# Kernel tuning notes

Hardware: AMD Instinct MI355X
Metric: run time of the kernel (lower is better)

The kernel has to match this reference:

```python
import jax, jax.numpy as jnp
import numpy as np

THETA = 0.5  # forward default arg
ALPHA = 0.2  # LeakyReLU negative slope
NEG_INF = -9e15


def setup_inputs() -> dict:
    key = jax.random.key(0)
    k1, k2, k3, k4, k5 = jax.random.split(key, 5)
    N, F_IN, F_OUT = 8192, 256, 256
    h = jax.random.normal(k1, (N, F_IN), dtype=jnp.float32)
    adj = jax.random.randint(k2, (N, N), 0, 2, dtype=jnp.int32)
    cv_values = jax.random.uniform(k3, (N,), dtype=jnp.float32)
    # xavier_uniform with gain=1.414
    g = 1.414
    bw = g * np.sqrt(6.0 / (F_IN + F_OUT))
    W = jax.random.uniform(k4, (F_IN, F_OUT), dtype=jnp.float32, minval=-bw, maxval=bw)
    ba = g * np.sqrt(6.0 / (2 * F_OUT + 1))
    a = jax.random.uniform(k5, (2 * F_OUT, 1), dtype=jnp.float32, minval=-ba, maxval=ba)
    return {"h": h, "adj": adj, "cv_values": cv_values, "W": W, "a": a}


def reference(h, adj, cv_values, W, a):
    # Wh: [N, F_out]
    Wh = h @ W
    F_out = Wh.shape[1]
    a1 = a[:F_out, 0]   # [F_out]
    a2 = a[F_out:, 0]   # [F_out]
    # e_ij = LeakyReLU([Wh_i ; Wh_j] . a) = LeakyReLU(Wh_i.a1 + Wh_j.a2)
    f1 = Wh @ a1        # [N]
    f2 = Wh @ a2        # [N]
    e = jax.nn.leaky_relu(f1[:, None] + f2[None, :], negative_slope=ALPHA)
    # CV bias: theta * cv_i broadcast across row i
    e = e + THETA * cv_values[:, None]
    att = jnp.where(adj > 0, e, jnp.float32(NEG_INF))
    att = jax.nn.softmax(att, axis=1)
    # dropout is identity in eval mode (training=False)
    h_prime = att @ Wh  # [N, F_out]
    return jax.nn.elu(h_prime)  # concat=True branch
```

## Files before the change

### kernel.cpp

```cpp
#include <hip/hip_runtime.h>
#include <cstdint>
#include <cstddef>

typedef _Float16 half8 __attribute__((ext_vector_type(8)));
typedef _Float16 half4 __attribute__((ext_vector_type(4)));
typedef float f32x4 __attribute__((ext_vector_type(4)));

#define GAT_N 8192
#define GAT_F 256
#define GAT_ALPHA 0.2f
#define GAT_LOG2E 1.4426950408889634f

__device__ inline unsigned enc_f32(float x) {
    unsigned b = __float_as_uint(x);
    return (b & 0x80000000u) ? ~b : (b | 0x80000000u);
}
__device__ inline float dec_f32(unsigned u) {
    unsigned b = (u & 0x80000000u) ? (u ^ 0x80000000u) : ~u;
    return __uint_as_float(b);
}

__global__ __launch_bounds__(256) void gat_k0_convert(
    const float* __restrict__ h, const float* __restrict__ W,
    _Float16* __restrict__ h16, _Float16* __restrict__ WT,
    unsigned* __restrict__ f2mxEnc)
{
    const int gtid = blockIdx.x * 256 + threadIdx.x;
    if (gtid == 0) *f2mxEnc = 0u;
    for (int i = gtid; i < (GAT_N * GAT_F / 4); i += 131072) {
        float4 v = reinterpret_cast<const float4*>(h)[i];
        half4 o; o[0] = (_Float16)v.x; o[1] = (_Float16)v.y;
        o[2] = (_Float16)v.z; o[3] = (_Float16)v.w;
        reinterpret_cast<half4*>(h16)[i] = o;
    }
    if (gtid < GAT_F * GAT_F) {
        int k = gtid >> 8, n = gtid & 255;
        WT[n * GAT_F + k] = (_Float16)W[gtid];
    }
}

__global__ __launch_bounds__(256) void gat_k1_gemm(
    const _Float16* __restrict__ h16, const _Float16* __restrict__ WT,
    const float* __restrict__ a, _Float16* __restrict__ whT,
    float* __restrict__ f1, float* __restrict__ f2,
    unsigned* __restrict__ f2mxEnc)
{
    const int wv = threadIdx.x >> 6;
    const int lane = threadIdx.x & 63;
    const int l15 = lane & 15;
    const int quad = lane >> 4;
    const int r0 = blockIdx.x * 64 + wv * 16;

    f32x4 acc[16];
    #pragma unroll
    for (int t = 0; t < 16; ++t) { f32x4 z = {0.f,0.f,0.f,0.f}; acc[t] = z; }

    #pragma unroll
    for (int k0 = 0; k0 < GAT_F; k0 += 32) {
        half8 af = *reinterpret_cast<const half8*>(
            h16 + (size_t)(r0 + l15) * GAT_F + k0 + quad * 8);
        #pragma unroll
        for (int t = 0; t < 16; ++t) {
            half8 bf = *reinterpret_cast<const half8*>(
                WT + (size_t)(t * 16 + l15) * GAT_F + k0 + quad * 8);
            acc[t] = __builtin_amdgcn_mfma_f32_16x16x32_f16(af, bf, acc[t], 0, 0, 0);
        }
    }

    float p1[4] = {0.f,0.f,0.f,0.f}, p2[4] = {0.f,0.f,0.f,0.f};
    #pragma unroll
    for (int t = 0; t < 16; ++t) {
        float a1c = a[t * 16 + l15];
        float a2c = a[GAT_F + t * 16 + l15];
        #pragma unroll
        for (int r = 0; r < 4; ++r) {
            p1[r] = fmaf(acc[t][r], a1c, p1[r]);
            p2[r] = fmaf(acc[t][r], a2c, p2[r]);
        }
    }
    #pragma unroll
    for (int off = 1; off < 16; off <<= 1) {
        #pragma unroll
        for (int r = 0; r < 4; ++r) {
            p1[r] += __shfl_xor(p1[r], off);
            p2[r] += __shfl_xor(p2[r], off);
        }
    }
    if (l15 == 0) {
        float mx = -3.0e38f;
        #pragma unroll
        for (int r = 0; r < 4; ++r) {
            int row = r0 + quad * 4 + r;
            f1[row] = p1[r];
            f2[row] = p2[r];
            mx = fmaxf(mx, p2[r]);
        }
        atomicMax(f2mxEnc, enc_f32(mx));
    }

    #pragma unroll
    for (int t = 0; t < 16; ++t) {
        half4 hv;
        #pragma unroll
        for (int r = 0; r < 4; ++r) hv[r] = (_Float16)acc[t][r];
        *reinterpret_cast<half4*>(
            whT + (size_t)(t * 16 + l15) * GAT_N + r0 + quad * 4) = hv;
    }
}

__global__ __launch_bounds__(256, 2) void gat_k3_attn(
    const int* __restrict__ adj, const float* __restrict__ f1,
    const float* __restrict__ f2, const unsigned* __restrict__ f2mxEnc,
    const _Float16* __restrict__ whT,
    _Float16* __restrict__ Ph,
    float* __restrict__ L)
{
    const int bx = blockIdx.x;
    const int rb = bx >> 3;
    const int q  = bx & 7;
    const int wv = threadIdx.x >> 6;
    const int lane = threadIdx.x & 63;
    const int l15 = lane & 15;
    const int quad = lane >> 4;

    const int r0 = rb * 128 + wv * 32;
    const int rA = r0 + l15;
    const int rB = r0 + 16 + l15;

    const float fmx = dec_f32(*f2mxEnc);
    const float f1A = f1[rA];
    const float f1B = f1[rB];
    const float sA = f1A + fmx;
    const float sB = f1B + fmx;
    const float CA = GAT_LOG2E * (fmaxf(sA, 0.f) + GAT_ALPHA * fminf(sA, 0.f));
    const float CB = GAT_LOG2E * (fmaxf(sB, 0.f) + GAT_ALPHA * fminf(sB, 0.f));

    f32x4 acc[2][16];
    #pragma unroll
    for (int s = 0; s < 2; ++s)
        #pragma unroll
        for (int t = 0; t < 16; ++t) {
            f32x4 z = {0.f,0.f,0.f,0.f};
            acc[s][t] = z;
        }
    float d0 = 0.f, d1 = 0.f;

    const int kq = q * 1024;
    const size_t rowA = (size_t)rA * GAT_N;
    const size_t rowB = (size_t)rB * GAT_N;
    const _Float16* wbase = whT + (size_t)l15 * GAT_N;

    int kb0 = kq + quad * 8;
    int4 nA0 = *reinterpret_cast<const int4*>(adj + rowA + kb0);
    int4 nA1 = *reinterpret_cast<const int4*>(adj + rowA + kb0 + 4);
    int4 nB0 = *reinterpret_cast<const int4*>(adj + rowB + kb0);
    int4 nB1 = *reinterpret_cast<const int4*>(adj + rowB + kb0 + 4);
    float4 nfa = *reinterpret_cast<const float4*>(f2 + kb0);
    float4 nfb = *reinterpret_cast<const float4*>(f2 + kb0 + 4);

    #pragma unroll 2
    for (int step = 0; step < 32; ++step) {
        const int4 cA0 = nA0, cA1 = nA1, cB0 = nB0, cB1 = nB1;
        const float4 cfa = nfa, cfb = nfb;
        if (step < 31) {
            const int kbn = kq + (step + 1) * 32 + quad * 8;
            nA0 = *reinterpret_cast<const int4*>(adj + rowA + kbn);
            nA1 = *reinterpret_cast<const int4*>(adj + rowA + kbn + 4);
            nB0 = *reinterpret_cast<const int4*>(adj + rowB + kbn);
            nB1 = *reinterpret_cast<const int4*>(adj + rowB + kbn + 4);
            nfa = *reinterpret_cast<const float4*>(f2 + kbn);
            nfb = *reinterpret_cast<const float4*>(f2 + kbn + 4);
        }

        const float f2v[8] = {cfa.x, cfa.y, cfa.z, cfa.w, cfb.x, cfb.y, cfb.z, cfb.w};
        const int am[8] = {cA0.x, cA0.y, cA0.z, cA0.w, cA1.x, cA1.y, cA1.z, cA1.w};
        const int bm[8] = {cB0.x, cB0.y, cB0.z, cB0.w, cB1.x, cB1.y, cB1.z, cB1.w};

        half8 pA, pB;
        #pragma unroll
        for (int j = 0; j < 8; ++j) {
            float f2j = f2v[j];
            float xa = f1A + f2j;
            float la = fmaxf(xa, 0.f) + GAT_ALPHA * fminf(xa, 0.f);
            float pa = __builtin_amdgcn_exp2f(fmaf(la, GAT_LOG2E, -CA));
            pa = (am[j] > 0) ? pa : 0.f;
            d0 += pa;
            pA[j] = (_Float16)pa;
            float xb = f1B + f2j;
            float lb = fmaxf(xb, 0.f) + GAT_ALPHA * fminf(xb, 0.f);
            float pb = __builtin_amdgcn_exp2f(fmaf(lb, GAT_LOG2E, -CB));
            pb = (bm[j] > 0) ? pb : 0.f;
            d1 += pb;
            pB[j] = (_Float16)pb;
        }

        const int kb = kq + step * 32 + quad * 8;
        #pragma unroll
        for (int t = 0; t < 16; ++t) {
            half8 bf = *reinterpret_cast<const half8*>(
                wbase + (size_t)t * 16 * GAT_N + kb);
            acc[0][t] = __builtin_amdgcn_mfma_f32_16x16x32_f16(pA, bf, acc[0][t], 0, 0, 0);
            acc[1][t] = __builtin_amdgcn_mfma_f32_16x16x32_f16(pB, bf, acc[1][t], 0, 0, 0);
        }
    }

    d0 += __shfl_xor(d0, 16); d0 += __shfl_xor(d0, 32);
    d1 += __shfl_xor(d1, 16); d1 += __shfl_xor(d1, 32);
    float* Lq = L + q * GAT_N;
    if (lane < 16) { Lq[rA] = d0; Lq[rB] = d1; }

    const int wid = rb * 4 + wv;
    _Float16* Pq = Ph + ((size_t)q * 256 + wid) * 8192;
    #pragma unroll
    for (int s = 0; s < 2; ++s)
        #pragma unroll
        for (int t = 0; t < 16; ++t) {
            half4 hv;
            #pragma unroll
            for (int r = 0; r < 4; ++r) hv[r] = (_Float16)acc[s][t][r];
            *reinterpret_cast<half4*>(Pq + (size_t)(((s * 16 + t) * 64 + lane) * 4)) = hv;
        }
}

__global__ __launch_bounds__(256) void gat_k4_final(
    const _Float16* __restrict__ Ph, const float* __restrict__ L,
    float* __restrict__ out)
{
    const int tid = threadIdx.x;
    const int wid = blockIdx.x >> 3;
    __shared__ float s_rl[32];
    if (tid < 32) {
        const int row = wid * 32 + tid;
        float s = 0.f;
        #pragma unroll
        for (int q = 0; q < 8; ++q) s += L[q * GAT_N + row];
        s_rl[tid] = 1.0f / fmaxf(s, 1e-30f);
    }
    __syncthreads();

    const int idx = blockIdx.x * 256 + tid;
    const int rem = idx & 2047;
    const int lane = rem & 63;
    const int st = rem >> 6;
    const int s = st >> 4, t = st & 15;
    const int l15 = lane & 15, quad = lane >> 4;
    const int lrow0 = s * 16 + quad * 4;
    const int col = t * 16 + l15;

    float accv[4] = {0.f, 0.f, 0.f, 0.f};
    #pragma unroll
    for (int q = 0; q < 8; ++q) {
        half4 v = *reinterpret_cast<const half4*>(
            Ph + ((size_t)q * 256 + wid) * 8192 + (size_t)rem * 4);
        #pragma unroll
        for (int r = 0; r < 4; ++r) accv[r] += (float)v[r];
    }
    #pragma unroll
    for (int r = 0; r < 4; ++r) {
        const float v = accv[r] * s_rl[lrow0 + r];
        const float o = v > 0.f ? v : expm1f(v);
        out[(size_t)(wid * 32 + lrow0 + r) * GAT_F + col] = o;
    }
}

extern "C" void kernel_launch(void* const* d_in, const int* in_sizes, int n_in,
                              void* d_out, int out_size, void* d_ws, size_t ws_size,
                              hipStream_t stream)
{
    const float* h   = (const float*)d_in[0];
    const int*   adj = (const int*)d_in[1];
    const float* W   = (const float*)d_in[3];
    const float* a   = (const float*)d_in[4];
    float* out = (float*)d_out;
    char* ws = (char*)d_ws;

    const size_t SLAB = (size_t)GAT_N * GAT_F * 2;

    _Float16* whT = (_Float16*)(ws);
    _Float16* Ph  = (_Float16*)(ws + SLAB);
    _Float16* h16 = Ph;
    _Float16* WT  = Ph + (SLAB / 2);
    char* tail = ws + SLAB + 8 * SLAB;
    float* f1 = (float*)(tail);
    float* f2 = (float*)(tail + GAT_N * 4);
    float* L  = (float*)(tail + 2 * GAT_N * 4);
    unsigned* f2mxEnc = (unsigned*)(tail + 2 * GAT_N * 4 + 8 * GAT_N * 4);

    gat_k0_convert<<<512, 256, 0, stream>>>(h, W, h16, WT, f2mxEnc);
    gat_k1_gemm<<<128, 256, 0, stream>>>(h16, WT, a, whT, f1, f2, f2mxEnc);
    gat_k3_attn<<<512, 256, 0, stream>>>(adj, f1, f2, f2mxEnc, whT, Ph, L);
    gat_k4_final<<<2048, 256, 0, stream>>>(Ph, L, out);
}
```

Baseline: 502.1 us.

## Pack adjacency into bitmask, fuse h conversion into GEMM, prescale logits by log2e

Adds a pre-pass that packs the int32 adjacency matrix into a bitmask, so the attention kernel reads one bit per neighbour instead of four bytes. The attention kernel is reworked to pull 128-bit words and extract per-quad byte masks. The fp32-to-fp16 conversion of h moves into the GEMM kernel, which now runs smaller blocks. f1/f2 are prescaled by log2e so the leaky-relu plus exp2 path needs fewer ops. The adjacency matrix is still read in full once by the pack pass, so the main saving is removing the adjacency traffic from the attention loop.

```diff
diff --git a/kernel.cpp b/kernel.cpp
--- a/kernel.cpp
+++ b/kernel.cpp
@@ -8,6 +8,7 @@
 
 #define GAT_N 8192
 #define GAT_F 256
+#define GAT_NW 256
 #define GAT_ALPHA 0.2f
 #define GAT_LOG2E 1.4426950408889634f
 
@@ -20,36 +21,47 @@
     return __uint_as_float(b);
 }
 
-__global__ __launch_bounds__(256) void gat_k0_convert(
-    const float* __restrict__ h, const float* __restrict__ W,
-    _Float16* __restrict__ h16, _Float16* __restrict__ WT,
+__global__ __launch_bounds__(256) void gat_k0_pack(
+    const int* __restrict__ adj, unsigned char* __restrict__ adjB)
+{
+    const int wv = threadIdx.x >> 6;
+    const int lane = threadIdx.x & 63;
+    const int row = blockIdx.x * 4 + wv;
+    const int* src = adj + (size_t)row * GAT_N;
+    unsigned char* dst = adjB + (size_t)row * (GAT_N / 8);
+    #pragma unroll 4
+    for (int k = 0; k < 16; ++k) {
+        const int4 v0 = *reinterpret_cast<const int4*>(src + k * 512 + lane * 8);
+        const int4 v1 = *reinterpret_cast<const int4*>(src + k * 512 + lane * 8 + 4);
+        unsigned m = (unsigned)(v0.x > 0)        | ((unsigned)(v0.y > 0) << 1)
+                   | ((unsigned)(v0.z > 0) << 2) | ((unsigned)(v0.w > 0) << 3)
+                   | ((unsigned)(v1.x > 0) << 4) | ((unsigned)(v1.y > 0) << 5)
+                   | ((unsigned)(v1.z > 0) << 6) | ((unsigned)(v1.w > 0) << 7);
+        dst[k * 64 + lane] = (unsigned char)m;
+    }
+}
+
+__global__ __launch_bounds__(256) void gat_k0b_convert(
+    const float* __restrict__ W, _Float16* __restrict__ WT,
     unsigned* __restrict__ f2mxEnc)
 {
-    const int gtid = blockIdx.x * 256 + threadIdx.x;
-    if (gtid == 0) *f2mxEnc = 0u;
-    for (int i = gtid; i < (GAT_N * GAT_F / 4); i += 131072) {
-        float4 v = reinterpret_cast<const float4*>(h)[i];
-        half4 o; o[0] = (_Float16)v.x; o[1] = (_Float16)v.y;
-        o[2] = (_Float16)v.z; o[3] = (_Float16)v.w;
-        reinterpret_cast<half4*>(h16)[i] = o;
-    }
-    if (gtid < GAT_F * GAT_F) {
-        int k = gtid >> 8, n = gtid & 255;
-        WT[n * GAT_F + k] = (_Float16)W[gtid];
-    }
-}
-
-__global__ __launch_bounds__(256) void gat_k1_gemm(
-    const _Float16* __restrict__ h16, const _Float16* __restrict__ WT,
+    const int g = blockIdx.x * 256 + threadIdx.x;
+    if (g == 0) *f2mxEnc = 0u;
+    const int k = g >> 8, n = g & 255;
+    WT[n * GAT_F + k] = (_Float16)W[g];
+}
+
+__global__ __launch_bounds__(128) void gat_k1_gemm(
+    const float* __restrict__ h, const _Float16* __restrict__ WT,
     const float* __restrict__ a, _Float16* __restrict__ whT,
-    float* __restrict__ f1, float* __restrict__ f2,
+    float* __restrict__ f1L, float* __restrict__ f2L,
     unsigned* __restrict__ f2mxEnc)
 {
     const int wv = threadIdx.x >> 6;
     const int lane = threadIdx.x & 63;
     const int l15 = lane & 15;
     const int quad = lane >> 4;
-    const int r0 = blockIdx.x * 64 + wv * 16;
+    const int r0 = blockIdx.x * 32 + wv * 16;
 
     f32x4 acc[16];
     #pragma unroll
@@ -57,8 +69,14 @@
 
     #pragma unroll
     for (int k0 = 0; k0 < GAT_F; k0 += 32) {
-        half8 af = *reinterpret_cast<const half8*>(
-            h16 + (size_t)(r0 + l15) * GAT_F + k0 + quad * 8);
+        const float* ap = h + (size_t)(r0 + l15) * GAT_F + k0 + quad * 8;
+        const float4 a0 = *reinterpret_cast<const float4*>(ap);
+        const float4 a1 = *reinterpret_cast<const float4*>(ap + 4);
+        half8 af;
+        af[0] = (_Float16)a0.x; af[1] = (_Float16)a0.y;
+        af[2] = (_Float16)a0.z; af[3] = (_Float16)a0.w;
+        af[4] = (_Float16)a1.x; af[5] = (_Float16)a1.y;
+        af[6] = (_Float16)a1.z; af[7] = (_Float16)a1.w;
         #pragma unroll
         for (int t = 0; t < 16; ++t) {
             half8 bf = *reinterpret_cast<const half8*>(
@@ -91,9 +109,11 @@
         #pragma unroll
         for (int r = 0; r < 4; ++r) {
             int row = r0 + quad * 4 + r;
-            f1[row] = p1[r];
-            f2[row] = p2[r];
-            mx = fmaxf(mx, p2[r]);
+            float s1 = p1[r] * GAT_LOG2E;
+            float s2 = p2[r] * GAT_LOG2E;
+            f1L[row] = s1;
+            f2L[row] = s2;
+            mx = fmaxf(mx, s2);
         }
         atomicMax(f2mxEnc, enc_f32(mx));
     }
@@ -109,8 +129,8 @@
 }
 
 __global__ __launch_bounds__(256, 2) void gat_k3_attn(
-    const int* __restrict__ adj, const float* __restrict__ f1,
-    const float* __restrict__ f2, const unsigned* __restrict__ f2mxEnc,
+    const unsigned* __restrict__ adjW, const float* __restrict__ f1L,
+    const float* __restrict__ f2L, const unsigned* __restrict__ f2mxEnc,
     const _Float16* __restrict__ whT,
     _Float16* __restrict__ Ph,
     float* __restrict__ L)
@@ -125,15 +145,15 @@
 
     const int r0 = rb * 128 + wv * 32;
     const int rA = r0 + l15;
-    const int rB = r0 + 16 + l15;
-
-    const float fmx = dec_f32(*f2mxEnc);
-    const float f1A = f1[rA];
-    const float f1B = f1[rB];
-    const float sA = f1A + fmx;
-    const float sB = f1B + fmx;
-    const float CA = GAT_LOG2E * (fmaxf(sA, 0.f) + GAT_ALPHA * fminf(sA, 0.f));
-    const float CB = GAT_LOG2E * (fmaxf(sB, 0.f) + GAT_ALPHA * fminf(sB, 0.f));
+    const int rB = rA + 16;
+
+    const float fmxL = dec_f32(*f2mxEnc);
+    const float f1A = f1L[rA];
+    const float f1B = f1L[rB];
+    const float sA = f1A + fmxL;
+    const float sB = f1B + fmxL;
+    const float CA = fmaxf(sA, GAT_ALPHA * sA);
+    const float CB = fmaxf(sB, GAT_ALPHA * sB);
 
     f32x4 acc[2][16];
     #pragma unroll
@@ -146,61 +166,60 @@
     float d0 = 0.f, d1 = 0.f;
 
     const int kq = q * 1024;
-    const size_t rowA = (size_t)rA * GAT_N;
-    const size_t rowB = (size_t)rB * GAT_N;
+    const uint4* awA = reinterpret_cast<const uint4*>(adjW + (size_t)rA * GAT_NW + q * 32);
+    const uint4* awB = reinterpret_cast<const uint4*>(adjW + (size_t)rB * GAT_NW + q * 32);
     const _Float16* wbase = whT + (size_t)l15 * GAT_N;
-
-    int kb0 = kq + quad * 8;
-    int4 nA0 = *reinterpret_cast<const int4*>(adj + rowA + kb0);
-    int4 nA1 = *reinterpret_cast<const int4*>(adj + rowA + kb0 + 4);
-    int4 nB0 = *reinterpret_cast<const int4*>(adj + rowB + kb0);
-    int4 nB1 = *reinterpret_cast<const int4*>(adj + rowB + kb0 + 4);
-    float4 nfa = *reinterpret_cast<const float4*>(f2 + kb0);
-    float4 nfb = *reinterpret_cast<const float4*>(f2 + kb0 + 4);
-
-    #pragma unroll 2
-    for (int step = 0; step < 32; ++step) {
-        const int4 cA0 = nA0, cA1 = nA1, cB0 = nB0, cB1 = nB1;
-        const float4 cfa = nfa, cfb = nfb;
-        if (step < 31) {
-            const int kbn = kq + (step + 1) * 32 + quad * 8;
-            nA0 = *reinterpret_cast<const int4*>(adj + rowA + kbn);
-            nA1 = *reinterpret_cast<const int4*>(adj + rowA + kbn + 4);
-            nB0 = *reinterpret_cast<const int4*>(adj + rowB + kbn);
-            nB1 = *reinterpret_cast<const int4*>(adj + rowB + kbn + 4);
-            nfa = *reinterpret_cast<const float4*>(f2 + kbn);
-            nfb = *reinterpret_cast<const float4*>(f2 + kbn + 4);
-        }
-
-        const float f2v[8] = {cfa.x, cfa.y, cfa.z, cfa.w, cfb.x, cfb.y, cfb.z, cfb.w};
-        const int am[8] = {cA0.x, cA0.y, cA0.z, cA0.w, cA1.x, cA1.y, cA1.z, cA1.w};
-        const int bm[8] = {cB0.x, cB0.y, cB0.z, cB0.w, cB1.x, cB1.y, cB1.z, cB1.w};
-
-        half8 pA, pB;
-        #pragma unroll
-        for (int j = 0; j < 8; ++j) {
-            float f2j = f2v[j];
-            float xa = f1A + f2j;
-            float la = fmaxf(xa, 0.f) + GAT_ALPHA * fminf(xa, 0.f);
-            float pa = __builtin_amdgcn_exp2f(fmaf(la, GAT_LOG2E, -CA));
-            pa = (am[j] > 0) ? pa : 0.f;
-            d0 += pa;
-            pA[j] = (_Float16)pa;
-            float xb = f1B + f2j;
-            float lb = fmaxf(xb, 0.f) + GAT_ALPHA * fminf(xb, 0.f);
-            float pb = __builtin_amdgcn_exp2f(fmaf(lb, GAT_LOG2E, -CB));
-            pb = (bm[j] > 0) ? pb : 0.f;
-            d1 += pb;
-            pB[j] = (_Float16)pb;
-        }
-
-        const int kb = kq + step * 32 + quad * 8;
-        #pragma unroll
-        for (int t = 0; t < 16; ++t) {
-            half8 bf = *reinterpret_cast<const half8*>(
-                wbase + (size_t)t * 16 * GAT_N + kb);
-            acc[0][t] = __builtin_amdgcn_mfma_f32_16x16x32_f16(pA, bf, acc[0][t], 0, 0, 0);
-            acc[1][t] = __builtin_amdgcn_mfma_f32_16x16x32_f16(pB, bf, acc[1][t], 0, 0, 0);
+    const float* f2q = f2L + kq + quad * 8;
+
+    uint4 nA = awA[0];
+    uint4 nB = awB[0];
+    float4 nfa = *reinterpret_cast<const float4*>(f2q);
+    float4 nfb = *reinterpret_cast<const float4*>(f2q + 4);
+
+    for (int g = 0; g < 8; ++g) {
+        const uint4 cA = nA, cB = nB;
+        if (g < 7) { nA = awA[g + 1]; nB = awB[g + 1]; }
+        const unsigned wordsA[4] = {cA.x, cA.y, cA.z, cA.w};
+        const unsigned wordsB[4] = {cB.x, cB.y, cB.z, cB.w};
+
+        #pragma unroll
+        for (int s4 = 0; s4 < 4; ++s4) {
+            const int step = g * 4 + s4;
+            const float4 cfa = nfa, cfb = nfb;
+            if (step < 31) {
+                nfa = *reinterpret_cast<const float4*>(f2q + (step + 1) * 32);
+                nfb = *reinterpret_cast<const float4*>(f2q + (step + 1) * 32 + 4);
+            }
+            const unsigned mA = (wordsA[s4] >> (quad * 8)) & 0xffu;
+            const unsigned mB = (wordsB[s4] >> (quad * 8)) & 0xffu;
+            const float f2v[8] = {cfa.x, cfa.y, cfa.z, cfa.w, cfb.x, cfb.y, cfb.z, cfb.w};
+
+            half8 pA, pB;
+            #pragma unroll
+            for (int j = 0; j < 8; ++j) {
+                const float f2j = f2v[j];
+                float xa = f1A + f2j;
+                float la = fmaxf(xa, GAT_ALPHA * xa);
+                float pa = __builtin_amdgcn_exp2f(la - CA);
+                pa = (mA & (1u << j)) ? pa : 0.f;
+                d0 += pa;
+                pA[j] = (_Float16)pa;
+                float xb = f1B + f2j;
+                float lb = fmaxf(xb, GAT_ALPHA * xb);
+                float pb = __builtin_amdgcn_exp2f(lb - CB);
+                pb = (mB & (1u << j)) ? pb : 0.f;
+                d1 += pb;
+                pB[j] = (_Float16)pb;
+            }
+
+            const int kb = kq + step * 32 + quad * 8;
+            #pragma unroll
+            for (int t = 0; t < 16; ++t) {
+                half8 bf = *reinterpret_cast<const half8*>(
+                    wbase + (size_t)t * 16 * GAT_N + kb);
+                acc[0][t] = __builtin_amdgcn_mfma_f32_16x16x32_f16(pA, bf, acc[0][t], 0, 0, 0);
+                acc[1][t] = __builtin_amdgcn_mfma_f32_16x16x32_f16(pB, bf, acc[1][t], 0, 0, 0);
+            }
         }
     }
 
@@ -276,18 +295,19 @@
 
     const size_t SLAB = (size_t)GAT_N * GAT_F * 2;
 
-    _Float16* whT = (_Float16*)(ws);
-    _Float16* Ph  = (_Float16*)(ws + SLAB);
-    _Float16* h16 = Ph;
-    _Float16* WT  = Ph + (SLAB / 2);
-    char* tail = ws + SLAB + 8 * SLAB;
-    float* f1 = (float*)(tail);
-    float* f2 = (float*)(tail + GAT_N * 4);
-    float* L  = (float*)(tail + 2 * GAT_N * 4);
-    unsigned* f2mxEnc = (unsigned*)(tail + 2 * GAT_N * 4 + 8 * GAT_N * 4);
-
-    gat_k0_convert<<<512, 256, 0, stream>>>(h, W, h16, WT, f2mxEnc);
-    gat_k1_gemm<<<128, 256, 0, stream>>>(h16, WT, a, whT, f1, f2, f2mxEnc);
-    gat_k3_attn<<<512, 256, 0, stream>>>(adj, f1, f2, f2mxEnc, whT, Ph, L);
+    size_t off = 0;
+    _Float16* whT = (_Float16*)(ws + off); off += SLAB;
+    _Float16* Ph  = (_Float16*)(ws + off); off += 8 * SLAB;
+    unsigned char* adjB = (unsigned char*)(ws + off); off += (size_t)GAT_N * GAT_N / 8;
+    _Float16* WT  = (_Float16*)(ws + off); off += (size_t)GAT_F * GAT_F * 2;
+    float* f1L = (float*)(ws + off); off += GAT_N * 4;
+    float* f2L = (float*)(ws + off); off += GAT_N * 4;
+    float* L   = (float*)(ws + off); off += 8 * GAT_N * 4;
+    unsigned* f2mxEnc = (unsigned*)(ws + off); off += 256;
+
+    gat_k0_pack<<<2048, 256, 0, stream>>>(adj, adjB);
+    gat_k0b_convert<<<256, 256, 0, stream>>>(W, WT, f2mxEnc);
+    gat_k1_gemm<<<256, 128, 0, stream>>>(h, WT, a, whT, f1L, f2L, f2mxEnc);
+    gat_k3_attn<<<512, 256, 0, stream>>>((const unsigned*)adjB, f1L, f2L, f2mxEnc, whT, Ph, L);
     gat_k4_final<<<2048, 256, 0, stream>>>(Ph, L, out);
 }
```

Result: slower. 579.0 us (+15.3%).
